# Optimization experiments

Measured on AMD Instinct MI355X. Metric: run time of the kernel, lower is better.

## Reference

```python
import jax, jax.numpy as jnp
import numpy as np

N = 100000      # nodes (single node type)
R = 4           # relations
E = 800000      # edges per relation (avg in-degree ~32)
D_IN, D_H, D_OUT = 256, 64, 16


def setup_inputs() -> dict:
    key = jax.random.key(0)
    ks = jax.random.split(key, 9)
    x = jax.random.normal(ks[0], (N, D_IN), dtype=jnp.float32)
    src = jax.random.randint(ks[1], (R, E), 0, N, dtype=jnp.int32)
    dst = jax.random.randint(ks[2], (R, E), 0, N, dtype=jnp.int32)
    s_in = 1.0 / np.sqrt(D_IN)
    s_h = 1.0 / np.sqrt(D_H)
    W1 = jax.random.normal(ks[3], (R, D_IN, D_H), dtype=jnp.float32) * s_in
    L1w = jax.random.normal(ks[4], (D_IN, D_H), dtype=jnp.float32) * s_in
    L1b = jnp.zeros((D_H,), dtype=jnp.float32)
    W2 = jax.random.normal(ks[5], (R, D_H, D_OUT), dtype=jnp.float32) * s_h
    L2w = jax.random.normal(ks[6], (D_H, D_OUT), dtype=jnp.float32) * s_h
    L2b = jnp.zeros((D_OUT,), dtype=jnp.float32)
    return {"x": x, "src": src, "dst": dst, "W1": W1, "L1w": L1w,
            "L1b": L1b, "W2": W2, "L2w": L2w, "L2b": L2b}


def _rel_graph_conv(h, src, dst, W):
    """Per-relation GEMM + gather + scatter-add + right-normalize, summed over relations.
    h: [N, d_in]; src/dst: [R, E]; W: [R, d_in, d_out] -> [N, d_out]
    """
    hw = jnp.einsum('nd,rdh->rnh', h, W)  # transform first (d_out small), then gather

    def agg(hr, s, d):
        deg = jax.ops.segment_sum(jnp.ones((E,), hr.dtype), d, num_segments=N)
        msg = jax.ops.segment_sum(hr[s], d, num_segments=N)  # [N, d_out]
        return msg / jnp.maximum(deg, 1.0)[:, None]          # norm='right'

    return jnp.sum(jax.vmap(agg)(hw, src, dst), axis=0)


def reference(x, src, dst, W1, L1w, L1b, W2, L2w, L2b):
    # Layer 1: relation conv + self-loop linear + ReLU (dropout = eval/identity)
    h = _rel_graph_conv(x, src, dst, W1) + x @ L1w + L1b
    h = jax.nn.relu(h)
    # Layer 2: no activation
    out = _rel_graph_conv(h, src, dst, W2) + h @ L2w + L2b
    return out
```

## Files before the change

### kernel.cpp

```cpp
#include <hip/hip_runtime.h>


constexpr int NN = 100000, RR = 4, EE = 800000;
constexpr int RE = RR * EE;
constexpr int NBKT = (NN + 63) / 64;
constexpr int BCAP = 3072;
constexpr int NCOARSE = 49;
constexpr int CCAP = 69632;
constexpr int NCH = 17;
constexpr int NG1 = (NN + 63) / 64;
constexpr int CHUNK = 4096;
constexpr int NB = (RE + CHUNK - 1) / CHUNK;
constexpr int EPT = CHUNK / 512;

typedef short bf16x8 __attribute__((ext_vector_type(8)));
typedef float f32x4 __attribute__((ext_vector_type(4)));

__device__ inline unsigned short f2bf(float f) {
  unsigned u = __float_as_uint(f);
  u += 0x7FFF + ((u >> 16) & 1);
  return (unsigned short)(u >> 16);
}
__device__ inline float bf2f(unsigned short s) {
  return __uint_as_float(((unsigned)s) << 16);
}

__global__ __launch_bounds__(256) void prep_w_kernel(const float* __restrict__ W1,
                                                     const float* __restrict__ L1w,
                                                     const float* __restrict__ W2,
                                                     const float* __restrict__ L2w,
                                                     unsigned short* __restrict__ BT1,
                                                     unsigned short* __restrict__ BT2) {
  int idx = blockIdx.x * 256 + threadIdx.x;
  if (idx < 320 * 256) {
    int n = idx >> 8, k = idx & 255;
    float v = (n < 256) ? W1[((size_t)((n >> 6) * 256 + k)) * 64 + (n & 63)]
                        : L1w[(size_t)k * 64 + (n - 256)];
    BT1[idx] = f2bf(v);
  } else {
    int j = idx - 320 * 256;
    if (j < 80 * 64) {
      int n = j >> 6, k = j & 63;
      float v = (n < 64) ? W2[((size_t)((n >> 4) * 64 + k)) * 16 + (n & 15)]
                         : L2w[(size_t)k * 16 + (n - 64)];
      BT2[j] = f2bf(v);
    }
  }
}

__global__ __launch_bounds__(512) void fused1_kernel(const float* __restrict__ x,
                                                     const unsigned short* __restrict__ BT1,
                                                     const float* __restrict__ L1b,
                                                     const int* __restrict__ src,
                                                     const int* __restrict__ dst,
                                                     int* __restrict__ gcoarse,
                                                     int* __restrict__ cbuf,
                                                     unsigned short* __restrict__ hwcat,
                                                     unsigned short* __restrict__ h) {
  __shared__ char lds[49152];
  const int bid = blockIdx.x;
  const int t = threadIdx.x;
  const bool is_bin = (bid % 3 == 0) && (bid / 3 < NB);

  if (is_bin) {
    int* hist = (int*)lds;
    int* cur = hist + 64;
    int* delta = cur + 64;
    int* sorted = delta + 64;
    unsigned char* cb = (unsigned char*)(sorted + 4096);
    const int fid = bid / 3;

    if (t < 64) hist[t] = 0;
    __syncthreads();
    const int e0 = fid * CHUNK + t;
    int dl[EPT], sl[EPT];
#pragma unroll
    for (int i = 0; i < EPT; ++i) {
      int fl = e0 + i * 512;
      dl[i] = -1;
      if (fl < RE) {
        dl[i] = dst[fl];
        sl[i] = src[fl];
        atomicAdd(&hist[dl[i] >> 11], 1);
      }
    }
    __syncthreads();
    if (t < 64) {
      int c = (t < NCOARSE) ? hist[t] : 0;
      int xs = c;
#pragma unroll
      for (int d = 1; d < 64; d <<= 1) {
        int y = __shfl_up(xs, d);
        if (t >= d) xs += y;
      }
      int excl = xs - c;
      if (t < NCOARSE) {
        cur[t] = excl;
        int gb = (c > 0) ? atomicAdd(&gcoarse[t], c) : 0;
        delta[t] = gb - excl;
      }
    }
    __syncthreads();
#pragma unroll
    for (int i = 0; i < EPT; ++i) {
      if (dl[i] < 0) continue;
      int fl = e0 + i * 512;
      int r = fl / EE;
      int cg = dl[i] >> 11;
      int p = atomicAdd(&cur[cg], 1);
      sorted[p] = (sl[i] << 2) | r | ((dl[i] & 2047) << 19);
      cb[p] = (unsigned char)cg;
    }
    __syncthreads();
    int ptot = RE - fid * CHUNK;
    if (ptot > CHUNK) ptot = CHUNK;
#pragma unroll
    for (int i = 0; i < EPT; ++i) {
      int p = t + i * 512;
      if (p < ptot) {
        int cg = cb[p];
        int inb = delta[cg] + p;
        if (inb < CCAP) cbuf[(size_t)cg * CCAP + inb] = sorted[p];
      }
    }
    return;
  }

  int nbins = (bid + 2) / 3;
  if (nbins > NB) nbins = NB;
  const int m0 = (bid - nbins) * 64;
  char* Al = lds;
  char* Bl = lds + 8192;
  const int wid = t >> 6, lane = t & 63;
  const int wm = wid >> 2, wn = wid & 3;
  const int l15 = lane & 15, g = lane >> 4;

  f32x4 acc[2][5];
#pragma unroll
  for (int i = 0; i < 2; ++i)
#pragma unroll
    for (int j = 0; j < 5; ++j) acc[i][j] = (f32x4){0.f, 0.f, 0.f, 0.f};

  for (int kc = 0; kc < 4; ++kc) {
    if (kc) __syncthreads();
#pragma unroll
    for (int it = 0; it < 2; ++it) {
      int fl = t + 512 * it;
      int row = fl >> 4, kq = (fl & 15) * 4;
      int rg = m0 + row;
      float4 v = (rg < NN) ? *(const float4*)(x + (size_t)rg * 256 + kc * 64 + kq)
                           : make_float4(0.f, 0.f, 0.f, 0.f);
      ushort4 pck = {f2bf(v.x), f2bf(v.y), f2bf(v.z), f2bf(v.w)};
      int wb = ((row * 64 + kq) * 2) ^ ((row & 7) << 4);
      *(ushort4*)(Al + wb) = pck;
    }
#pragma unroll
    for (int it = 0; it < 5; ++it) {
      int fl = t + 512 * it;
      int n = fl >> 3, i8 = (fl & 7) * 8;
      uint4 u = *(const uint4*)(BT1 + (size_t)n * 256 + kc * 64 + i8);
      int wb = ((n * 64 + i8) * 2) ^ ((n & 7) << 4);
      *(uint4*)(Bl + wb) = u;
    }
    __syncthreads();
#pragma unroll
    for (int ks = 0; ks < 2; ++ks) {
      bf16x8 af[2], bfr[5];
#pragma unroll
      for (int mi = 0; mi < 2; ++mi) {
        int row = wm * 32 + mi * 16 + l15;
        int byte = ((row * 64 + ks * 32 + g * 8) * 2) ^ ((row & 7) << 4);
        af[mi] = *(const bf16x8*)(Al + byte);
      }
#pragma unroll
      for (int ni = 0; ni < 5; ++ni) {
        int n = wn * 80 + ni * 16 + l15;
        int byte = ((n * 64 + ks * 32 + g * 8) * 2) ^ ((n & 7) << 4);
        bfr[ni] = *(const bf16x8*)(Bl + byte);
      }
#pragma unroll
      for (int mi = 0; mi < 2; ++mi)
#pragma unroll
        for (int ni = 0; ni < 5; ++ni)
          acc[mi][ni] = __builtin_amdgcn_mfma_f32_16x16x32_bf16(af[mi], bfr[ni], acc[mi][ni], 0, 0, 0);
    }
  }
#pragma unroll
  for (int mi = 0; mi < 2; ++mi) {
    int rbase = m0 + wm * 32 + mi * 16 + 4 * g;
#pragma unroll
    for (int ni = 0; ni < 5; ++ni) {
      int n0 = wn * 80 + ni * 16;
      int n = n0 + l15;
#pragma unroll
      for (int e = 0; e < 4; ++e) {
        int row = rbase + e;
        if (row >= NN) continue;
        float v = acc[mi][ni][e];
        if (n0 < 256) hwcat[(size_t)row * 256 + n] = f2bf(v);
        else h[(size_t)row * 64 + (n - 256)] = f2bf(v + L1b[n - 256]);
      }
    }
  }
}

__global__ __launch_bounds__(512) void pass2_kernel(const int* __restrict__ cbuf,
                                                    const int* __restrict__ gcoarse,
                                                    int* __restrict__ gcur,
                                                    int* __restrict__ binned) {
  __shared__ int hist32[32], cur32[32], delta32[32];
  __shared__ int sorted[4096];
  __shared__ unsigned char cb[4096];
  const int t = threadIdx.x;
  const int g = blockIdx.x / NCH, ch = blockIdx.x % NCH;
  int count = gcoarse[g];
  if (count > CCAP) count = CCAP;
  const int base = ch * 4096;
  int nhere = count - base;
  if (nhere <= 0) return;
  if (nhere > 4096) nhere = 4096;

  if (t < 32) hist32[t] = 0;
  __syncthreads();
  int wl[8], fl8[8];
#pragma unroll
  for (int i = 0; i < 8; ++i) {
    int j = t + i * 512;
    fl8[i] = -1;
    if (j < nhere) {
      int w = cbuf[(size_t)g * CCAP + base + j];
      wl[i] = w;
      fl8[i] = (w >> 25) & 31;
      atomicAdd(&hist32[fl8[i]], 1);
    }
  }
  __syncthreads();
  if (t < 32) {
    int c = hist32[t];
    int xs = c;
#pragma unroll
    for (int d = 1; d < 32; d <<= 1) {
      int y = __shfl_up(xs, d);
      if (t >= d) xs += y;
    }
    int excl = xs - c;
    cur32[t] = excl;
    int gb = (c > 0) ? atomicAdd(&gcur[g * 32 + t], c) : 0;
    delta32[t] = gb - excl;
  }
  __syncthreads();
#pragma unroll
  for (int i = 0; i < 8; ++i) {
    if (fl8[i] < 0) continue;
    int p = atomicAdd(&cur32[fl8[i]], 1);
    int w = wl[i];
    sorted[p] = (w & 0x7FFFF) | (((w >> 19) & 63) << 19);
    cb[p] = (unsigned char)fl8[i];
  }
  __syncthreads();
#pragma unroll
  for (int i = 0; i < 8; ++i) {
    int p = t + i * 512;
    if (p < nhere) {
      int f = cb[p];
      int inb = delta32[f] + p;
      if (inb < BCAP) binned[(size_t)(g * 32 + f) * BCAP + inb] = sorted[p];
    }
  }
}

__global__ __launch_bounds__(256) void pull1_kernel(const unsigned short* __restrict__ h,
                                                    const unsigned short* __restrict__ hwcat,
                                                    const int* __restrict__ binned,
                                                    const int* __restrict__ gcur,
                                                    const unsigned short* __restrict__ BT2,
                                                    const float* __restrict__ L2b,
                                                    unsigned short* __restrict__ hw2,
                                                    float* __restrict__ out) {
  __shared__ int csr[BCAP];
  __shared__ int cnt[256];
  __shared__ int off[256];
  __shared__ float winv[256];
  __shared__ int tot[64];
  __shared__ char Al[64 * 64 * 2];
  const int t = threadIdx.x, bkt = blockIdx.x;
  const int wid = t >> 6, lane = t & 63;
  const int l15 = lane & 15, g = lane >> 4;

  int count = gcur[bkt];
  if (count > BCAP) count = BCAP;
  const int* edges = binned + (size_t)bkt * BCAP;

  cnt[t] = 0;
  __syncthreads();
  for (int i = t; i < count; i += 256) {
    int w = edges[i];
    atomicAdd(&cnt[((w >> 19) & 63) * 4 + (w & 3)], 1);
  }
  __syncthreads();
  off[t] = cnt[t];
  __syncthreads();
  for (int s = 1; s < 256; s <<= 1) {
    int v = (t >= s) ? off[t - s] : 0;
    __syncthreads();
    off[t] += v;
    __syncthreads();
  }
  int excl = off[t] - cnt[t];
  winv[t] = 1.0f / (float)(cnt[t] > 1 ? cnt[t] : 1);
  __syncthreads();
  off[t] = excl;
  cnt[t] = excl;
  __syncthreads();
  if (t < 64) tot[t] = ((t == 63) ? count : off[(t + 1) * 4]) - off[t * 4];
  __syncthreads();
  for (int i = t; i < count; i += 256) {
    int w = edges[i];
    int k = ((w >> 19) & 63) * 4 + (w & 3);
    int p = atomicAdd(&cnt[k], 1);
    csr[p] = w & 0x7FFFF;
  }
  __syncthreads();

  const int slot = lane >> 3, cpart = lane & 7;
  for (int ii = 0; ii < 16; ++ii) {
    int nloc = wid * 16 + ii;
    int beg = off[nloc * 4];
    int total = tot[nloc];
    float acc[8] = {0.f, 0.f, 0.f, 0.f, 0.f, 0.f, 0.f, 0.f};
    for (int p0 = 0; p0 < total; p0 += 8) {
      int j = p0 + slot;
      bool pr = j < total;
      int key = pr ? csr[beg + j] : 0;
      float wv = pr ? winv[nloc * 4 + (key & 3)] : 0.f;
      uint4 u = *(const uint4*)(hwcat + (size_t)key * 64 + cpart * 8);
#pragma unroll
      for (int q = 0; q < 4; ++q) {
        unsigned uu = (&u.x)[q];
        acc[q * 2]     = fmaf(wv, bf2f((unsigned short)(uu & 0xffffu)), acc[q * 2]);
        acc[q * 2 + 1] = fmaf(wv, bf2f((unsigned short)(uu >> 16)), acc[q * 2 + 1]);
      }
    }
#pragma unroll
    for (int m = 8; m <= 32; m <<= 1)
#pragma unroll
      for (int q = 0; q < 8; ++q) acc[q] += __shfl_xor(acc[q], m);
    if (slot == 0) {
      int gn = bkt * 64 + nloc;
      unsigned pk[4];
      uint4 hu = make_uint4(0, 0, 0, 0);
      if (gn < NN) hu = *(const uint4*)(h + (size_t)gn * 64 + cpart * 8);
#pragma unroll
      for (int q = 0; q < 4; ++q) {
        unsigned a = (&hu.x)[q];
        float v0 = acc[q * 2]     + bf2f((unsigned short)(a & 0xffffu));
        float v1 = acc[q * 2 + 1] + bf2f((unsigned short)(a >> 16));
        pk[q] = (unsigned)f2bf(fmaxf(v0, 0.f)) | ((unsigned)f2bf(fmaxf(v1, 0.f)) << 16);
      }
      int wb = ((nloc * 64 + cpart * 8) * 2) ^ ((nloc & 7) << 4);
      *(uint4*)(Al + wb) = make_uint4(pk[0], pk[1], pk[2], pk[3]);
    }
  }
  __syncthreads();

  char* Bl = (char*)csr;
#pragma unroll
  for (int it = 0; it < 3; ++it) {
    int fl = t + 256 * it;
    if (fl < 640) {
      int n = fl >> 3, i8 = (fl & 7) * 8;
      uint4 u = *(const uint4*)(BT2 + (size_t)n * 64 + i8);
      int wb = ((n * 64 + i8) * 2) ^ ((n & 7) << 4);
      *(uint4*)(Bl + wb) = u;
    }
  }
  __syncthreads();

  f32x4 acc2[5];
#pragma unroll
  for (int j = 0; j < 5; ++j) acc2[j] = (f32x4){0.f, 0.f, 0.f, 0.f};
#pragma unroll
  for (int ks = 0; ks < 2; ++ks) {
    int ra = wid * 16 + l15;
    int byte = ((ra * 64 + ks * 32 + g * 8) * 2) ^ ((ra & 7) << 4);
    bf16x8 af = *(const bf16x8*)(Al + byte);
#pragma unroll
    for (int ni = 0; ni < 5; ++ni) {
      int n = ni * 16 + l15;
      int nb = ((n * 64 + ks * 32 + g * 8) * 2) ^ ((n & 7) << 4);
      bf16x8 bfr = *(const bf16x8*)(Bl + nb);
      acc2[ni] = __builtin_amdgcn_mfma_f32_16x16x32_bf16(af, bfr, acc2[ni], 0, 0, 0);
    }
  }
  int rb = wid * 16 + 4 * g;
#pragma unroll
  for (int ni = 0; ni < 5; ++ni) {
    int n0 = ni * 16;
    int n = n0 + l15;
#pragma unroll
    for (int e = 0; e < 4; ++e) {
      int gno = bkt * 64 + rb + e;
      if (gno >= NN) continue;
      float vv = acc2[ni][e];
      if (n0 < 64) hw2[(size_t)gno * 64 + n] = f2bf(vv);
      else out[(size_t)gno * 16 + (n - 64)] = vv + L2b[n - 64];
    }
  }
}

__global__ __launch_bounds__(256) void pull2_kernel(const unsigned short* __restrict__ hw2,
                                                    const int* __restrict__ binned,
                                                    const int* __restrict__ gcur,
                                                    float* __restrict__ out) {
  __shared__ int csr[BCAP];
  __shared__ int cnt[256];
  __shared__ int off[256];
  __shared__ float winv[256];
  __shared__ int tot[64];
  __shared__ float ot[64][16];
  const int t = threadIdx.x, bkt = blockIdx.x;
  const int wid = t >> 6, lane = t & 63;

  int count = gcur[bkt];
  if (count > BCAP) count = BCAP;
  const int* edges = binned + (size_t)bkt * BCAP;

  cnt[t] = 0;
  __syncthreads();
  for (int i = t; i < count; i += 256) {
    int w = edges[i];
    atomicAdd(&cnt[((w >> 19) & 63) * 4 + (w & 3)], 1);
  }
  __syncthreads();
  off[t] = cnt[t];
  __syncthreads();
  for (int s = 1; s < 256; s <<= 1) {
    int v = (t >= s) ? off[t - s] : 0;
    __syncthreads();
    off[t] += v;
    __syncthreads();
  }
  int excl = off[t] - cnt[t];
  winv[t] = 1.0f / (float)(cnt[t] > 1 ? cnt[t] : 1);
  __syncthreads();
  off[t] = excl;
  cnt[t] = excl;
  __syncthreads();
  if (t < 64) tot[t] = ((t == 63) ? count : off[(t + 1) * 4]) - off[t * 4];
  __syncthreads();
  for (int i = t; i < count; i += 256) {
    int w = edges[i];
    int k = ((w >> 19) & 63) * 4 + (w & 3);
    int p = atomicAdd(&cnt[k], 1);
    csr[p] = w & 0x7FFFF;
  }
  __syncthreads();

  const int slot = lane >> 2, cpart = lane & 3;
  for (int ii = 0; ii < 16; ++ii) {
    int nloc = wid * 16 + ii;
    int beg = off[nloc * 4];
    int total = tot[nloc];
    float acc[4] = {0.f, 0.f, 0.f, 0.f};
    for (int p0 = 0; p0 < total; p0 += 16) {
      int j = p0 + slot;
      bool pr = j < total;
      int key = pr ? csr[beg + j] : 0;
      float wv = pr ? winv[nloc * 4 + (key & 3)] : 0.f;
      uint2 u = *(const uint2*)(hw2 + (size_t)key * 16 + cpart * 4);
      acc[0] = fmaf(wv, bf2f((unsigned short)(u.x & 0xffffu)), acc[0]);
      acc[1] = fmaf(wv, bf2f((unsigned short)(u.x >> 16)), acc[1]);
      acc[2] = fmaf(wv, bf2f((unsigned short)(u.y & 0xffffu)), acc[2]);
      acc[3] = fmaf(wv, bf2f((unsigned short)(u.y >> 16)), acc[3]);
    }
#pragma unroll
    for (int m = 4; m <= 32; m <<= 1)
#pragma unroll
      for (int q = 0; q < 4; ++q) acc[q] += __shfl_xor(acc[q], m);
    if (slot == 0)
      *(float4*)&ot[nloc][cpart * 4] = make_float4(acc[0], acc[1], acc[2], acc[3]);
  }
  __syncthreads();

  int row = t >> 2, q = t & 3;
  int gn = bkt * 64 + row;
  if (gn < NN) {
    float4 o = *(float4*)(out + (size_t)gn * 16 + q * 4);
    float4 a = *(float4*)&ot[row][q * 4];
    o.x += a.x; o.y += a.y; o.z += a.z; o.w += a.w;
    *(float4*)(out + (size_t)gn * 16 + q * 4) = o;
  }
}

extern "C" void kernel_launch(void* const* d_in, const int* in_sizes, int n_in,
                              void* d_out, int out_size, void* d_ws, size_t ws_size,
                              hipStream_t stream) {
  const float* x   = (const float*)d_in[0];
  const int*   src = (const int*)d_in[1];
  const int*   dst = (const int*)d_in[2];
  const float* W1  = (const float*)d_in[3];
  const float* L1w = (const float*)d_in[4];
  const float* L1b = (const float*)d_in[5];
  const float* W2  = (const float*)d_in[6];
  const float* L2w = (const float*)d_in[7];
  const float* L2b = (const float*)d_in[8];
  float* out = (float*)d_out;

  char* p = (char*)d_ws;
  int* binned = (int*)p;                      p += (size_t)NBKT * BCAP * 4;
  int* gcur   = (int*)p;                      p += 49 * 32 * 4;
  int* gcoarse = (int*)p;                     p += 64 * 4;
  int* cbuf   = (int*)p;                      p += (size_t)NCOARSE * CCAP * 4;
  unsigned short* hwcat = (unsigned short*)p; p += (size_t)NN * 256 * 2;
  unsigned short* h = (unsigned short*)p;     p += (size_t)NN * 64 * 2;
  unsigned short* hw2 = (unsigned short*)p;   p += (size_t)NN * 64 * 2;
  unsigned short* BT1 = (unsigned short*)p;   p += 320 * 256 * 2;
  unsigned short* BT2 = (unsigned short*)p;   p += 80 * 64 * 2;
  if ((size_t)(p - (char*)d_ws) > ws_size) return;

  hipMemsetAsync(gcur, 0, (49 * 32 + 64) * 4, stream);
  prep_w_kernel<<<(320 * 256 + 80 * 64 + 255) / 256, 256, 0, stream>>>(W1, L1w, W2, L2w, BT1, BT2);
  fused1_kernel<<<NG1 + NB, 512, 0, stream>>>(x, BT1, L1b, src, dst, gcoarse, cbuf, hwcat, h);
  pass2_kernel<<<NCOARSE * NCH, 512, 0, stream>>>(cbuf, gcoarse, gcur, binned);
  pull1_kernel<<<NBKT, 256, 0, stream>>>(h, hwcat, binned, gcur, BT2, L2b, hw2, out);
  pull2_kernel<<<NBKT, 256, 0, stream>>>(hw2, binned, gcur, out);
}
```

Baseline: 233.4 us.

## Reuse pull1's per-bucket CSR in pull2, wave-scan prefix sum, gather two nodes at once

pull1 now writes its sorted per-bucket CSR back into the binned buffer, together with per-node offset/count headers and inverse degrees. pull2 loads these directly instead of redoing the histogram, scan and counting sort. The block-wide prefix scan becomes a wavefront shuffle scan plus a 4-entry combine. The gather loop handles two destination nodes per iteration to keep more loads in flight. The cost is extra global writes and reads of the CSR, plus higher register pressure in pull1.

```diff
diff --git a/kernel.cpp b/kernel.cpp
--- a/kernel.cpp
+++ b/kernel.cpp
@@ -271,10 +271,12 @@
 
 __global__ __launch_bounds__(256) void pull1_kernel(const unsigned short* __restrict__ h,
                                                     const unsigned short* __restrict__ hwcat,
-                                                    const int* __restrict__ binned,
+                                                    int* __restrict__ binned,
                                                     const int* __restrict__ gcur,
                                                     const unsigned short* __restrict__ BT2,
                                                     const float* __restrict__ L2b,
+                                                    unsigned* __restrict__ hdrG,
+                                                    float* __restrict__ winvG,
                                                     unsigned short* __restrict__ hw2,
                                                     float* __restrict__ out) {
   __shared__ int csr[BCAP];
@@ -282,6 +284,7 @@
   __shared__ int off[256];
   __shared__ float winv[256];
   __shared__ int tot[64];
+  __shared__ int wsum[4];
   __shared__ char Al[64 * 64 * 2];
   const int t = threadIdx.x, bkt = blockIdx.x;
   const int wid = t >> 6, lane = t & 63;
@@ -298,22 +301,25 @@
     atomicAdd(&cnt[((w >> 19) & 63) * 4 + (w & 3)], 1);
   }
   __syncthreads();
-  off[t] = cnt[t];
-  __syncthreads();
-  for (int s = 1; s < 256; s <<= 1) {
-    int v = (t >= s) ? off[t - s] : 0;
-    __syncthreads();
-    off[t] += v;
-    __syncthreads();
-  }
-  int excl = off[t] - cnt[t];
-  winv[t] = 1.0f / (float)(cnt[t] > 1 ? cnt[t] : 1);
-  __syncthreads();
+  int v = cnt[t];
+  int xs = v;
+#pragma unroll
+  for (int d = 1; d < 64; d <<= 1) {
+    int y = __shfl_up(xs, d);
+    if (lane >= d) xs += y;
+  }
+  if (lane == 63) wsum[wid] = xs;
+  __syncthreads();
+  int add = 0;
+#pragma unroll
+  for (int w2 = 0; w2 < 4; ++w2)
+    if (w2 < wid) add += wsum[w2];
+  int excl = xs + add - v;
+  winv[t] = 1.0f / (float)(v > 1 ? v : 1);
   off[t] = excl;
   cnt[t] = excl;
   __syncthreads();
   if (t < 64) tot[t] = ((t == 63) ? count : off[(t + 1) * 4]) - off[t * 4];
-  __syncthreads();
   for (int i = t; i < count; i += 256) {
     int w = edges[i];
     int k = ((w >> 19) & 63) * 4 + (w & 3);
@@ -322,43 +328,62 @@
   }
   __syncthreads();
 
+  for (int i = t; i < count; i += 256) binned[(size_t)bkt * BCAP + i] = csr[i];
+  winvG[bkt * 256 + t] = winv[t];
+  if (t < 64) hdrG[bkt * 64 + t] = (unsigned)off[t * 4] | ((unsigned)tot[t] << 16);
+
   const int slot = lane >> 3, cpart = lane & 7;
-  for (int ii = 0; ii < 16; ++ii) {
-    int nloc = wid * 16 + ii;
-    int beg = off[nloc * 4];
-    int total = tot[nloc];
-    float acc[8] = {0.f, 0.f, 0.f, 0.f, 0.f, 0.f, 0.f, 0.f};
-    for (int p0 = 0; p0 < total; p0 += 8) {
+  for (int ii = 0; ii < 16; ii += 2) {
+    int nA = wid * 16 + ii, nB = nA + 1;
+    int begA = off[nA * 4], totA = tot[nA];
+    int begB = off[nB * 4], totB = tot[nB];
+    int tmax = totA > totB ? totA : totB;
+    float accA[8] = {0.f, 0.f, 0.f, 0.f, 0.f, 0.f, 0.f, 0.f};
+    float accB[8] = {0.f, 0.f, 0.f, 0.f, 0.f, 0.f, 0.f, 0.f};
+    for (int p0 = 0; p0 < tmax; p0 += 8) {
       int j = p0 + slot;
-      bool pr = j < total;
-      int key = pr ? csr[beg + j] : 0;
-      float wv = pr ? winv[nloc * 4 + (key & 3)] : 0.f;
-      uint4 u = *(const uint4*)(hwcat + (size_t)key * 64 + cpart * 8);
+      bool prA = j < totA, prB = j < totB;
+      int keyA = prA ? csr[begA + j] : 0;
+      int keyB = prB ? csr[begB + j] : 0;
+      float wvA = prA ? winv[nA * 4 + (keyA & 3)] : 0.f;
+      float wvB = prB ? winv[nB * 4 + (keyB & 3)] : 0.f;
+      uint4 uA = *(const uint4*)(hwcat + (size_t)keyA * 64 + cpart * 8);
+      uint4 uB = *(const uint4*)(hwcat + (size_t)keyB * 64 + cpart * 8);
 #pragma unroll
       for (int q = 0; q < 4; ++q) {
-        unsigned uu = (&u.x)[q];
-        acc[q * 2]     = fmaf(wv, bf2f((unsigned short)(uu & 0xffffu)), acc[q * 2]);
-        acc[q * 2 + 1] = fmaf(wv, bf2f((unsigned short)(uu >> 16)), acc[q * 2 + 1]);
+        unsigned a = (&uA.x)[q], b = (&uB.x)[q];
+        accA[q * 2]     = fmaf(wvA, bf2f((unsigned short)(a & 0xffffu)), accA[q * 2]);
+        accA[q * 2 + 1] = fmaf(wvA, bf2f((unsigned short)(a >> 16)), accA[q * 2 + 1]);
+        accB[q * 2]     = fmaf(wvB, bf2f((unsigned short)(b & 0xffffu)), accB[q * 2]);
+        accB[q * 2 + 1] = fmaf(wvB, bf2f((unsigned short)(b >> 16)), accB[q * 2 + 1]);
       }
     }
 #pragma unroll
     for (int m = 8; m <= 32; m <<= 1)
 #pragma unroll
-      for (int q = 0; q < 8; ++q) acc[q] += __shfl_xor(acc[q], m);
+      for (int q = 0; q < 8; ++q) {
+        accA[q] += __shfl_xor(accA[q], m);
+        accB[q] += __shfl_xor(accB[q], m);
+      }
     if (slot == 0) {
-      int gn = bkt * 64 + nloc;
-      unsigned pk[4];
-      uint4 hu = make_uint4(0, 0, 0, 0);
-      if (gn < NN) hu = *(const uint4*)(h + (size_t)gn * 64 + cpart * 8);
-#pragma unroll
-      for (int q = 0; q < 4; ++q) {
-        unsigned a = (&hu.x)[q];
-        float v0 = acc[q * 2]     + bf2f((unsigned short)(a & 0xffffu));
-        float v1 = acc[q * 2 + 1] + bf2f((unsigned short)(a >> 16));
-        pk[q] = (unsigned)f2bf(fmaxf(v0, 0.f)) | ((unsigned)f2bf(fmaxf(v1, 0.f)) << 16);
-      }
-      int wb = ((nloc * 64 + cpart * 8) * 2) ^ ((nloc & 7) << 4);
-      *(uint4*)(Al + wb) = make_uint4(pk[0], pk[1], pk[2], pk[3]);
+#pragma unroll
+      for (int s2 = 0; s2 < 2; ++s2) {
+        int nloc = s2 ? nB : nA;
+        const float* ac = s2 ? accB : accA;
+        int gn = bkt * 64 + nloc;
+        unsigned pk[4];
+        uint4 hu = make_uint4(0, 0, 0, 0);
+        if (gn < NN) hu = *(const uint4*)(h + (size_t)gn * 64 + cpart * 8);
+#pragma unroll
+        for (int q = 0; q < 4; ++q) {
+          unsigned a = (&hu.x)[q];
+          float v0 = ac[q * 2]     + bf2f((unsigned short)(a & 0xffffu));
+          float v1 = ac[q * 2 + 1] + bf2f((unsigned short)(a >> 16));
+          pk[q] = (unsigned)f2bf(fmaxf(v0, 0.f)) | ((unsigned)f2bf(fmaxf(v1, 0.f)) << 16);
+        }
+        int wb = ((nloc * 64 + cpart * 8) * 2) ^ ((nloc & 7) << 4);
+        *(uint4*)(Al + wb) = make_uint4(pk[0], pk[1], pk[2], pk[3]);
+      }
     }
   }
   __syncthreads();
@@ -411,62 +436,38 @@
 __global__ __launch_bounds__(256) void pull2_kernel(const unsigned short* __restrict__ hw2,
                                                     const int* __restrict__ binned,
                                                     const int* __restrict__ gcur,
+                                                    const unsigned* __restrict__ hdrG,
+                                                    const float* __restrict__ winvG,
                                                     float* __restrict__ out) {
   __shared__ int csr[BCAP];
-  __shared__ int cnt[256];
-  __shared__ int off[256];
-  __shared__ float winv[256];
-  __shared__ int tot[64];
+  __shared__ float winvL[256];
+  __shared__ int begL[64], totL[64];
   __shared__ float ot[64][16];
   const int t = threadIdx.x, bkt = blockIdx.x;
   const int wid = t >> 6, lane = t & 63;
 
   int count = gcur[bkt];
   if (count > BCAP) count = BCAP;
-  const int* edges = binned + (size_t)bkt * BCAP;
-
-  cnt[t] = 0;
-  __syncthreads();
-  for (int i = t; i < count; i += 256) {
-    int w = edges[i];
-    atomicAdd(&cnt[((w >> 19) & 63) * 4 + (w & 3)], 1);
-  }
-  __syncthreads();
-  off[t] = cnt[t];
-  __syncthreads();
-  for (int s = 1; s < 256; s <<= 1) {
-    int v = (t >= s) ? off[t - s] : 0;
-    __syncthreads();
-    off[t] += v;
-    __syncthreads();
-  }
-  int excl = off[t] - cnt[t];
-  winv[t] = 1.0f / (float)(cnt[t] > 1 ? cnt[t] : 1);
-  __syncthreads();
-  off[t] = excl;
-  cnt[t] = excl;
-  __syncthreads();
-  if (t < 64) tot[t] = ((t == 63) ? count : off[(t + 1) * 4]) - off[t * 4];
-  __syncthreads();
-  for (int i = t; i < count; i += 256) {
-    int w = edges[i];
-    int k = ((w >> 19) & 63) * 4 + (w & 3);
-    int p = atomicAdd(&cnt[k], 1);
-    csr[p] = w & 0x7FFFF;
+  for (int i = t; i < count; i += 256) csr[i] = binned[(size_t)bkt * BCAP + i];
+  winvL[t] = winvG[bkt * 256 + t];
+  if (t < 64) {
+    unsigned hd = hdrG[bkt * 64 + t];
+    begL[t] = hd & 0xffff;
+    totL[t] = hd >> 16;
   }
   __syncthreads();
 
   const int slot = lane >> 2, cpart = lane & 3;
   for (int ii = 0; ii < 16; ++ii) {
     int nloc = wid * 16 + ii;
-    int beg = off[nloc * 4];
-    int total = tot[nloc];
+    int beg = begL[nloc];
+    int total = totL[nloc];
     float acc[4] = {0.f, 0.f, 0.f, 0.f};
     for (int p0 = 0; p0 < total; p0 += 16) {
       int j = p0 + slot;
       bool pr = j < total;
       int key = pr ? csr[beg + j] : 0;
-      float wv = pr ? winv[nloc * 4 + (key & 3)] : 0.f;
+      float wv = pr ? winvL[nloc * 4 + (key & 3)] : 0.f;
       uint2 u = *(const uint2*)(hw2 + (size_t)key * 16 + cpart * 4);
       acc[0] = fmaf(wv, bf2f((unsigned short)(u.x & 0xffffu)), acc[0]);
       acc[1] = fmaf(wv, bf2f((unsigned short)(u.x >> 16)), acc[1]);
@@ -516,12 +517,14 @@
   unsigned short* hw2 = (unsigned short*)p;   p += (size_t)NN * 64 * 2;
   unsigned short* BT1 = (unsigned short*)p;   p += 320 * 256 * 2;
   unsigned short* BT2 = (unsigned short*)p;   p += 80 * 64 * 2;
+  unsigned* hdrG = (unsigned*)p;              p += (size_t)NBKT * 64 * 4;
+  float* winvG = (float*)p;                   p += (size_t)NBKT * 256 * 4;
   if ((size_t)(p - (char*)d_ws) > ws_size) return;
 
   hipMemsetAsync(gcur, 0, (49 * 32 + 64) * 4, stream);
   prep_w_kernel<<<(320 * 256 + 80 * 64 + 255) / 256, 256, 0, stream>>>(W1, L1w, W2, L2w, BT1, BT2);
   fused1_kernel<<<NG1 + NB, 512, 0, stream>>>(x, BT1, L1b, src, dst, gcoarse, cbuf, hwcat, h);
   pass2_kernel<<<NCOARSE * NCH, 512, 0, stream>>>(cbuf, gcoarse, gcur, binned);
-  pull1_kernel<<<NBKT, 256, 0, stream>>>(h, hwcat, binned, gcur, BT2, L2b, hw2, out);
-  pull2_kernel<<<NBKT, 256, 0, stream>>>(hw2, binned, gcur, out);
-}
+  pull1_kernel<<<NBKT, 256, 0, stream>>>(h, hwcat, binned, gcur, BT2, L2b, hdrG, winvG, hw2, out);
+  pull2_kernel<<<NBKT, 256, 0, stream>>>(hw2, binned, gcur, hdrG, winvG, out);
+}
```

Measured after the change: 225.8 us. 1.03x faster.
